# Optimization experiments

Hardware: AMD Instinct MI355X
Metric: run time of the kernel (lower is better)

The kernel has to match this reference:

```python
import jax, jax.numpy as jnp
import numpy as np

NUM_SAMPLES = 50

def _sample_bezier(cp, t):
    # cp: [4, 2], t: [S, 1] -> [S, 2]
    p0, p1, p2, p3 = cp[0], cp[1], cp[2], cp[3]
    return ((1 - t) ** 3 * p0 + 3 * (1 - t) ** 2 * t * p1
            + 3 * (1 - t) * t ** 2 * p2 + t ** 3 * p3)

def setup_inputs() -> dict:
    key = jax.random.key(0)
    k1, k2, k3 = jax.random.split(key, 3)
    num_strokes = 64
    return {
        "strokes": jax.random.uniform(k1, (num_strokes, 4, 2), dtype=jnp.float32),
        "stroke_widths": jax.random.uniform(k2, (num_strokes,), dtype=jnp.float32) * 2.0 + 1.0,
        "stroke_colors": jax.random.uniform(k3, (num_strokes, 3), dtype=jnp.float32),
        "canvas_size": 512,
    }

def reference(strokes, stroke_widths, stroke_colors, canvas_size):
    H = W = canvas_size
    t = jnp.linspace(0.0, 1.0, NUM_SAMPLES, dtype=strokes.dtype)[:, None]  # [S,1]
    # sample all curves: [num_strokes, S, 2], scaled to pixel coords
    points = jax.vmap(lambda cp: _sample_bezier(cp, t))(strokes) * canvas_size
    coords = jnp.arange(canvas_size, dtype=strokes.dtype)
    yy, xx = jnp.meshgrid(coords, coords, indexing="ij")
    grid = jnp.stack([xx, yy], axis=-1)  # [H, W, 2]

    def composite(canvas, inp):
        pts, width, color = inp  # [S,2], [], [3]
        diff = grid[:, :, None, :] - pts[None, None, :, :]      # [H, W, S, 2]
        dist = jnp.sqrt(jnp.sum(diff * diff, axis=-1))           # [H, W, S]
        min_dist = jnp.min(dist, axis=-1)                        # [H, W]
        alpha = jax.nn.sigmoid((width - min_dist) * 2.0)         # [H, W]
        alpha = alpha[None, None]                                # [1,1,H,W]
        color_map = color[None, :, None, None]                   # [1,3,1,1]
        canvas = canvas * (1.0 - alpha) + color_map * alpha
        return canvas, None

    canvas0 = jnp.ones((1, 3, H, W), dtype=strokes.dtype)
    canvas, _ = jax.lax.scan(composite, canvas0, (points, stroke_widths, stroke_colors))
    return canvas
```

## Files before the change

### kernel.cpp

```cpp
#include <hip/hip_runtime.h>

#define NSTROKES 64
#define NSAMP    50
#define CANVAS   512
#define HW       (CANVAS * CANVAS)
#define TPB      1024
#define SPW      (NSTROKES / 16)
#define LSTRIDE  64

__global__ __launch_bounds__(TPB, 8) void raster_fused_kernel(
    const float* __restrict__ strokes,
    const float* __restrict__ widths,
    const float* __restrict__ colors,
    float* __restrict__ out)
{
    __shared__ __align__(16) float2 slist[NSTROKES * LSTRIDE];
    __shared__ float4 scull[NSTROKES];
    __shared__ float4 scol [NSTROKES];
    __shared__ float4 xfer [512];

    const int tid  = threadIdx.x;
    const int wave = tid >> 6;
    const int lane = tid & 63;
    const int px   = tid & 511;
    const int grp  = tid >> 9;
    const int y    = blockIdx.x;
    const float fy = (float)y;

    #pragma unroll
    for (int i = 0; i < SPW; ++i) {
        const int s = wave * SPW + i;

        float4 a = ((const float4*)strokes)[s * 2];
        float4 b = ((const float4*)strokes)[s * 2 + 1];
        const float S = (float)CANVAS;
        float c0x = a.x * S;
        float c1x = 3.0f * (a.z - a.x) * S;
        float c2x = 3.0f * (b.x - 2.0f * a.z + a.x) * S;
        float c3x = (b.z - 3.0f * b.x + 3.0f * a.z - a.x) * S;
        float c0y = a.y * S;
        float c1y = 3.0f * (a.w - a.y) * S;
        float c2y = 3.0f * (b.y - 2.0f * a.w + a.y) * S;
        float c3y = (b.w - 3.0f * b.y + 3.0f * a.w - a.y) * S;

        float w   = widths[s];
        float cut = w + 10.0f;

        float t   = (float)lane * (1.0f / (float)(NSAMP - 1));
        float px_ = fmaf(fmaf(fmaf(c3x, t, c2x), t, c1x), t, c0x);
        float py_ = fmaf(fmaf(fmaf(c3y, t, c2y), t, c1y), t, c0y);

        float dy  = py_ - fy;
        bool keep = (lane < NSAMP) && (fabsf(dy) <= cut);
        unsigned long long mask = __ballot(keep);
        int idx = __popcll(mask & ((1ull << lane) - 1ull));
        if (keep) {
            slist[s * LSTRIDE + idx] = make_float2(px_, dy * dy);
        } else if (lane >= NSAMP) {
            slist[s * LSTRIDE + idx + (lane - NSAMP)] = make_float2(1e15f, 1e15f);
        }

        if (mask) {
            float vmn = keep ? px_ : 1e30f;
            float vmx = keep ? px_ : -1e30f;
            #pragma unroll
            for (int off = 32; off; off >>= 1) {
                vmn = fminf(vmn, __shfl_xor(vmn, off));
                vmx = fmaxf(vmx, __shfl_xor(vmx, off));
            }
            if (lane == 0) {
                scull[s] = make_float4(vmn - cut, vmx + cut, w,
                                       (float)__popcll(mask));
                scol [s] = make_float4(colors[3*s], colors[3*s+1],
                                       colors[3*s+2], 0.0f);
            }
        } else if (lane == 0) {
            scull[s] = make_float4(0.0f, 0.0f, w, 0.0f);
        }
    }
    __syncthreads();

    const float fx      = (float)px;
    const float span_lo = (float)((wave & 7) << 6);
    const float span_hi = span_lo + 63.0f;
    const int   sbase   = grp << 5;

    float4 cbl = scull[sbase + (lane & 31)];
    bool alive = (cbl.w > 0.0f) && (cbl.x <= span_hi) && (cbl.y >= span_lo);
    unsigned int live = (unsigned int)__ballot(alive);

    float A = 1.0f, br = 0.0f, bg = 0.0f, bb = 0.0f;

    while (live) {
        const int s0 = sbase + (__ffs(live) - 1);
        live &= live - 1u;
        const bool has1 = (live != 0u);
        const int s1 = has1 ? (sbase + (__ffs(live) - 1)) : s0;
        if (has1) live &= live - 1u;

        float4 cb0  = scull[s0];
        float4 cb1  = scull[s1];
        float4 col0 = scol [s0];
        float4 col1 = scol [s1];
        const int   kc0 = (int)cb0.w;
        const int   kc1 = has1 ? (int)cb1.w : 0;
        const float w0  = cb0.z;
        const float w1  = cb1.z;

        float m0 = 1e30f, m1 = 1e30f;
        const float4* L0 = (const float4*)(slist + s0 * LSTRIDE);
        const float4* L1 = (const float4*)(slist + s1 * LSTRIDE);

        const int kmax = kc0 > kc1 ? kc0 : kc1;
        for (int j = 0; j < kmax; j += 4) {
            if (j < kc0) {
                float4 q0 = L0[(j >> 1)];
                float4 q1 = L0[(j >> 1) + 1];
                float d0 = fx - q0.x, d1 = fx - q0.z;
                float d2 = fx - q1.x, d3 = fx - q1.z;
                float a01 = fminf(fmaf(d0, d0, q0.y), fmaf(d1, d1, q0.w));
                float a23 = fminf(fmaf(d2, d2, q1.y), fmaf(d3, d3, q1.w));
                m0 = fminf(fminf(a01, a23), m0);
            }
            if (j < kc1) {
                float4 q0 = L1[(j >> 1)];
                float4 q1 = L1[(j >> 1) + 1];
                float d0 = fx - q0.x, d1 = fx - q0.z;
                float d2 = fx - q1.x, d3 = fx - q1.z;
                float a01 = fminf(fmaf(d0, d0, q0.y), fmaf(d1, d1, q0.w));
                float a23 = fminf(fmaf(d2, d2, q1.y), fmaf(d3, d3, q1.w));
                m1 = fminf(fminf(a01, a23), m1);
            }
        }

        float al0 = __builtin_amdgcn_rcpf(1.0f + __expf(2.0f * (sqrtf(m0) - w0)));
        float al1 = __builtin_amdgcn_rcpf(1.0f + __expf(2.0f * (sqrtf(m1) - w1)));

        A  *= (1.0f - al0);
        br  = fmaf(al0, col0.x - br, br);
        bg  = fmaf(al0, col0.y - bg, bg);
        bb  = fmaf(al0, col0.z - bb, bb);
        if (has1) {
            A  *= (1.0f - al1);
            br  = fmaf(al1, col1.x - br, br);
            bg  = fmaf(al1, col1.y - bg, bg);
            bb  = fmaf(al1, col1.z - bb, bb);
        }
    }

    if (grp == 0) {
        xfer[px] = make_float4(A, br, bg, bb);
    }
    __syncthreads();
    if (grp == 1) {
        float4 g0 = xfer[px];
        float cr = fmaf(A, g0.x + g0.y, br);
        float cg = fmaf(A, g0.x + g0.z, bg);
        float cb = fmaf(A, g0.x + g0.w, bb);
        const int base = y * CANVAS + px;
        out[0*HW + base] = cr;
        out[1*HW + base] = cg;
        out[2*HW + base] = cb;
    }
}

extern "C" void kernel_launch(void* const* d_in, const int* in_sizes, int n_in,
                              void* d_out, int out_size, void* d_ws, size_t ws_size,
                              hipStream_t stream) {
    const float* strokes = (const float*)d_in[0];
    const float* widths  = (const float*)d_in[1];
    const float* colors  = (const float*)d_in[2];
    float* out = (float*)d_out;

    raster_fused_kernel<<<dim3(CANVAS), dim3(TPB), 0, stream>>>(
        strokes, widths, colors, out);
}
```

Baseline: 17.31 us.

## Precompute Bezier samples in a separate kernel and skip far-away stroke compositing

Result: slower. 22.38 us (+29.3%).

```diff
diff --git a/kernel.cpp b/kernel.cpp
--- a/kernel.cpp
+++ b/kernel.cpp
@@ -7,9 +7,41 @@
 #define TPB      1024
 #define SPW      (NSTROKES / 16)
 #define LSTRIDE  64
-
-__global__ __launch_bounds__(TPB, 8) void raster_fused_kernel(
+#define WS_NEED  ((size_t)NSTROKES * 64 * sizeof(float2))
+
+__global__ __launch_bounds__(256) void sample_kernel(
     const float* __restrict__ strokes,
+    float2* __restrict__ ws_pts)
+{
+    const int t = blockIdx.x * 256 + threadIdx.x;
+    const int s = t >> 6;
+    const int j = t & 63;
+
+    if (j >= NSAMP) {
+        ws_pts[t] = make_float2(1e15f, 1e15f);
+        return;
+    }
+
+    float4 a = ((const float4*)strokes)[s * 2];
+    float4 b = ((const float4*)strokes)[s * 2 + 1];
+    const float S = (float)CANVAS;
+    float c0x = a.x * S;
+    float c1x = 3.0f * (a.z - a.x) * S;
+    float c2x = 3.0f * (b.x - 2.0f * a.z + a.x) * S;
+    float c3x = (b.z - 3.0f * b.x + 3.0f * a.z - a.x) * S;
+    float c0y = a.y * S;
+    float c1y = 3.0f * (a.w - a.y) * S;
+    float c2y = 3.0f * (b.y - 2.0f * a.w + a.y) * S;
+    float c3y = (b.w - 3.0f * b.y + 3.0f * a.w - a.y) * S;
+
+    float tt = (float)j * (1.0f / (float)(NSAMP - 1));
+    float px = fmaf(fmaf(fmaf(c3x, tt, c2x), tt, c1x), tt, c0x);
+    float py = fmaf(fmaf(fmaf(c3y, tt, c2y), tt, c1y), tt, c0y);
+    ws_pts[t] = make_float2(px, py);
+}
+
+__global__ __launch_bounds__(TPB, 8) void raster_kernel(
+    const float2* __restrict__ ws_pts,
     const float* __restrict__ widths,
     const float* __restrict__ colors,
     float* __restrict__ out)
@@ -31,6 +63,148 @@
     for (int i = 0; i < SPW; ++i) {
         const int s = wave * SPW + i;
 
+        float2 q  = ws_pts[(s << 6) | lane];
+        float  w  = widths[s];
+        float cut = w + 10.0f;
+
+        float dy  = q.y - fy;
+        bool keep = fabsf(dy) <= cut;
+        unsigned long long mask = __ballot(keep);
+        int idx = __popcll(mask & ((1ull << lane) - 1ull));
+        if (keep) {
+            slist[s * LSTRIDE + idx] = make_float2(q.x, dy * dy);
+        } else if (lane >= NSAMP) {
+            slist[s * LSTRIDE + idx + (lane - NSAMP)] = make_float2(1e15f, 1e15f);
+        }
+
+        if (mask) {
+            float vmn = keep ? q.x : 1e30f;
+            float vmx = keep ? q.x : -1e30f;
+            #pragma unroll
+            for (int off = 32; off; off >>= 1) {
+                vmn = fminf(vmn, __shfl_xor(vmn, off));
+                vmx = fmaxf(vmx, __shfl_xor(vmx, off));
+            }
+            if (lane == 0) {
+                scull[s] = make_float4(vmn - cut, vmx + cut, w,
+                                       (float)__popcll(mask));
+                scol [s] = make_float4(colors[3*s], colors[3*s+1],
+                                       colors[3*s+2], 0.0f);
+            }
+        } else if (lane == 0) {
+            scull[s] = make_float4(0.0f, 0.0f, w, 0.0f);
+        }
+    }
+    __syncthreads();
+
+    const float fx      = (float)px;
+    const float span_lo = (float)((wave & 7) << 6);
+    const float span_hi = span_lo + 63.0f;
+    const int   sbase   = grp << 5;
+
+    float4 cbl = scull[sbase + (lane & 31)];
+    bool alive = (cbl.w > 0.0f) && (cbl.x <= span_hi) && (cbl.y >= span_lo);
+    unsigned int live = (unsigned int)__ballot(alive);
+
+    float A = 1.0f, br = 0.0f, bg = 0.0f, bb = 0.0f;
+
+    while (live) {
+        const int s0 = sbase + (__ffs(live) - 1);
+        live &= live - 1u;
+        const bool has1 = (live != 0u);
+        const int s1 = has1 ? (sbase + (__ffs(live) - 1)) : s0;
+        if (has1) live &= live - 1u;
+
+        float4 cb0  = scull[s0];
+        float4 cb1  = scull[s1];
+        float4 col0 = scol [s0];
+        float4 col1 = scol [s1];
+        const int   kc0 = (int)cb0.w;
+        const int   kc1 = has1 ? (int)cb1.w : 0;
+        const float w0  = cb0.z;
+        const float w1  = cb1.z;
+
+        float m0 = 1e30f, m1 = 1e30f;
+        const float4* L0 = (const float4*)(slist + s0 * LSTRIDE);
+        const float4* L1 = (const float4*)(slist + s1 * LSTRIDE);
+
+        const int kmax = kc0 > kc1 ? kc0 : kc1;
+        for (int j = 0; j < kmax; j += 4) {
+            if (j < kc0) {
+                float4 q0 = L0[(j >> 1)];
+                float4 q1 = L0[(j >> 1) + 1];
+                float d0 = fx - q0.x, d1 = fx - q0.z;
+                float d2 = fx - q1.x, d3 = fx - q1.z;
+                float a01 = fminf(fmaf(d0, d0, q0.y), fmaf(d1, d1, q0.w));
+                float a23 = fminf(fmaf(d2, d2, q1.y), fmaf(d3, d3, q1.w));
+                m0 = fminf(fminf(a01, a23), m0);
+            }
+            if (j < kc1) {
+                float4 q0 = L1[(j >> 1)];
+                float4 q1 = L1[(j >> 1) + 1];
+                float d0 = fx - q0.x, d1 = fx - q0.z;
+                float d2 = fx - q1.x, d3 = fx - q1.z;
+                float a01 = fminf(fmaf(d0, d0, q0.y), fmaf(d1, d1, q0.w));
+                float a23 = fminf(fmaf(d2, d2, q1.y), fmaf(d3, d3, q1.w));
+                m1 = fminf(fminf(a01, a23), m1);
+            }
+        }
+
+        const float c0 = w0 + 10.0f;
+        const float c1 = w1 + 10.0f;
+        if (__all(m0 > c0 * c0) && __all(m1 > c1 * c1)) continue;
+
+        float al0 = __builtin_amdgcn_rcpf(1.0f + __expf(2.0f * (sqrtf(m0) - w0)));
+        float al1 = __builtin_amdgcn_rcpf(1.0f + __expf(2.0f * (sqrtf(m1) - w1)));
+
+        A  *= (1.0f - al0);
+        br  = fmaf(al0, col0.x - br, br);
+        bg  = fmaf(al0, col0.y - bg, bg);
+        bb  = fmaf(al0, col0.z - bb, bb);
+        if (has1) {
+            A  *= (1.0f - al1);
+            br  = fmaf(al1, col1.x - br, br);
+            bg  = fmaf(al1, col1.y - bg, bg);
+            bb  = fmaf(al1, col1.z - bb, bb);
+        }
+    }
+
+    if (grp == 0) {
+        xfer[px] = make_float4(A, br, bg, bb);
+    }
+    __syncthreads();
+    if (grp == 1) {
+        float4 g0 = xfer[px];
+        float cr = fmaf(A, g0.x + g0.y, br);
+        float cg = fmaf(A, g0.x + g0.z, bg);
+        float cb = fmaf(A, g0.x + g0.w, bb);
+        const int base = y * CANVAS + px;
+        out[0*HW + base] = cr;
+        out[1*HW + base] = cg;
+        out[2*HW + base] = cb;
+    }
+}
+
+__global__ __launch_bounds__(TPB, 8) void raster_fused_fallback(
+    const float* __restrict__ strokes, const float* __restrict__ widths,
+    const float* __restrict__ colors, float* __restrict__ out)
+{
+    __shared__ __align__(16) float2 slist[NSTROKES * LSTRIDE];
+    __shared__ float4 scull[NSTROKES];
+    __shared__ float4 scol [NSTROKES];
+    __shared__ float4 xfer [512];
+
+    const int tid  = threadIdx.x;
+    const int wave = tid >> 6;
+    const int lane = tid & 63;
+    const int px   = tid & 511;
+    const int grp  = tid >> 9;
+    const int y    = blockIdx.x;
+    const float fy = (float)y;
+
+    #pragma unroll
+    for (int i = 0; i < SPW; ++i) {
+        const int s = wave * SPW + i;
         float4 a = ((const float4*)strokes)[s * 2];
         float4 b = ((const float4*)strokes)[s * 2 + 1];
         const float S = (float)CANVAS;
@@ -172,6 +346,14 @@
     const float* colors  = (const float*)d_in[2];
     float* out = (float*)d_out;
 
-    raster_fused_kernel<<<dim3(CANVAS), dim3(TPB), 0, stream>>>(
-        strokes, widths, colors, out);
+    if (ws_size >= WS_NEED) {
+        float2* ws_pts = (float2*)d_ws;
+        sample_kernel<<<dim3((NSTROKES * 64) / 256), dim3(256), 0, stream>>>(
+            strokes, ws_pts);
+        raster_kernel<<<dim3(CANVAS), dim3(TPB), 0, stream>>>(
+            ws_pts, widths, colors, out);
+    } else {
+        raster_fused_fallback<<<dim3(CANVAS), dim3(TPB), 0, stream>>>(
+            strokes, widths, colors, out);
+    }
 }
```
